# Kernel optimization log

Measured on AMD Instinct MI355X. Metric: run time of the kernel, lower is better.

Reference implementation:

```python
import jax, jax.numpy as jnp
import numpy as np
from jax.scipy.special import logsumexp

# Model config: alphabet='ACGTZY', collapse='ACGTCA' -> 4 canonical bases, 2 mods
NBASE = 4
NTRANS = 2 * NBASE * (NBASE + 1)          # 40 flip-flop transition states
CAN_NMODS = np.array([1, 1, 0, 0])        # mods per canonical base (A:Y, C:Z)
SIZE = NTRANS + 1 + int(CAN_NMODS.sum())  # 43 linear outputs
LARGE_LOG_VAL = np.float32(50000.0)
T, N, INSIZE = 2000, 128, 256


def _can_indices():
    """Per-canonical-base index groups into the mod block of the linear output."""
    idx, cur = [], 0
    for nm in CAN_NMODS:
        idx.append(np.concatenate([[0], np.arange(cur + 1, cur + 1 + nm)]))
        cur += nm
    return idx

CAN_INDICES = _can_indices()


def setup_inputs() -> dict:
    key = jax.random.key(0)
    k1, k2, k3 = jax.random.split(key, 3)
    x = jax.random.normal(k1, (T, N, INSIZE), dtype=jnp.float32)
    W = jax.random.normal(k2, (SIZE, INSIZE), dtype=jnp.float32) / np.float32(INSIZE ** 0.5)
    b = jax.random.normal(k3, (SIZE,), dtype=jnp.float32) * 0.1
    return {"x": x, "W": W, "b": b}


def global_norm_flipflop(scores):
    """Log-partition of the flip-flop CRF via a sequential log-space scan.

    scores: (T, N, 2*nbase*(nbase+1)).
    """
    Tn, Nn, _ = scores.shape
    # initial state: flip states uniform, flop states ~ -inf
    fwd0 = jnp.concatenate(
        [jnp.zeros((Nn, NBASE), scores.dtype),
         jnp.full((Nn, NBASE), -LARGE_LOG_VAL, scores.dtype)], axis=1)
    logZ0 = logsumexp(fwd0, axis=1, keepdims=True)
    fwd0 = fwd0 - logZ0

    def step(carry, scores_t):
        fwd, logZ = carry
        # (N, nbase+1, 2*nbase): dest-state x source-state transition scores
        curr = fwd[:, None, :] + scores_t.reshape(Nn, NBASE + 1, 2 * NBASE)
        base1 = logsumexp(curr[:, :NBASE], axis=2)                    # to-flip states
        base2 = jnp.logaddexp(curr[:, NBASE, :NBASE],
                              curr[:, NBASE, NBASE:])                 # to-flop (stay)
        new = jnp.concatenate([base1, base2], axis=1)                 # (N, 2*nbase)
        fac = logsumexp(new, axis=1, keepdims=True)
        return (new - fac, logZ + fac), None

    (_, logZ), _ = jax.lax.scan(step, (fwd0, logZ0), scores)
    return scores - logZ / np.float32(Tn)


def reference(x, W, b):
    # Linear projection: (T, N, insize) -> (T, N, size)
    y = jnp.einsum('tnf,cf->tnc', x, W) + b
    # Globally-normalized flip-flop transition scores
    trans = global_norm_flipflop(y[:, :, :NTRANS])
    # Per-canonical-base categorical (can + its mods) log-softmax scores
    mods = [jax.nn.log_softmax(y[:, :, NTRANS + idx], axis=2) for idx in CAN_INDICES]
    return jnp.concatenate([trans] + mods, axis=2)
```

## Files before the change

### kernel.cpp

```cpp
#include <hip/hip_runtime.h>

#define T_DIM 2000
#define N_DIM 128
#define IN_DIM 256
#define OUT_C 46
#define NROWS (T_DIM * N_DIM)
#define NCHUNK 250
#define CLEN 8
#define NSUPER 25
#define SLEN 10

typedef short bf16x8 __attribute__((ext_vector_type(8)));
typedef float f32x4 __attribute__((ext_vector_type(4)));

union F8U { bf16x8 v; uint32_t u[4]; };

__device__ __forceinline__ uint32_t cvtpk(float lo, float hi) {
  uint32_t r;
  asm("v_cvt_pk_bf16_f32 %0, %1, %2" : "=v"(r) : "v"(lo), "v"(hi));
  return r;
}

__device__ __forceinline__ float bf2f(unsigned short u) {
  uint32_t w = (uint32_t)u << 16;
  return __builtin_bit_cast(float, w);
}

#define LDSK 264

__global__ __launch_bounds__(256, 4) void k1_gemm(const float* __restrict__ x,
                                                  const float* __restrict__ W,
                                                  const float* __restrict__ b,
                                                  unsigned short* __restrict__ wsYT,
                                                  float* __restrict__ wsMod) {
  __shared__ unsigned short Wl[43 * LDSK];
  const int tid  = threadIdx.x;
  const int lane = tid & 63;
  const int wv   = tid >> 6;
  const int ln   = lane & 15;
  const int lh   = lane >> 4;

  {
    uint32_t* Wd = reinterpret_cast<uint32_t*>(Wl);
#pragma unroll
    for (int it = 0; it < 22; ++it) {
      int e = tid + it * 256;
      if (e < 43 * 128) {
        int n = e >> 7, kp = e & 127;
        float2 w = *reinterpret_cast<const float2*>(W + (size_t)n * IN_DIM + 2 * kp);
        Wd[n * (LDSK / 2) + kp] = cvtpk(w.x, w.y);
      }
    }
  }
  float bias[3];
#pragma unroll
  for (int nt = 0; nt < 3; ++nt) {
    int n = nt * 16 + ln;
    bias[nt] = b[n > 42 ? 42 : n];
  }
  __syncthreads();

  const int rowbase = blockIdx.x * 256 + wv * 64;
  const float* xbase = x + (size_t)(rowbase + ln) * IN_DIM + lh * 8;

  float4 bufA[8], bufB[8];
  f32x4 zero = {0.f, 0.f, 0.f, 0.f};
  f32x4 acc[3] = {zero, zero, zero};

#define LOADH(BUF, T, HF) do {                                               \
    const float* _p = xbase + (size_t)(T) * (16 * IN_DIM) + (HF) * 128;      \
    _Pragma("unroll")                                                        \
    for (int _s = 0; _s < 4; ++_s) {                                         \
      BUF[_s]     = *reinterpret_cast<const float4*>(_p + _s * 32);          \
      BUF[_s + 4] = *reinterpret_cast<const float4*>(_p + _s * 32 + 4);      \
    }                                                                        \
  } while (0)

#define COMPH(BUF, HF) do {                                                  \
    _Pragma("unroll")                                                        \
    for (int _s2 = 0; _s2 < 4; ++_s2) {                                      \
      F8U _af;                                                               \
      _af.u[0] = cvtpk(BUF[_s2].x, BUF[_s2].y);                              \
      _af.u[1] = cvtpk(BUF[_s2].z, BUF[_s2].w);                              \
      _af.u[2] = cvtpk(BUF[_s2 + 4].x, BUF[_s2 + 4].y);                      \
      _af.u[3] = cvtpk(BUF[_s2 + 4].z, BUF[_s2 + 4].w);                      \
      const int _s = (HF) * 4 + _s2;                                         \
      _Pragma("unroll")                                                      \
      for (int _nt = 0; _nt < 3; ++_nt) {                                    \
        const bf16x8 _bf = *reinterpret_cast<const bf16x8*>(                 \
            &Wl[(_nt * 16 + ln) * LDSK + _s * 32 + lh * 8]);                 \
        acc[_nt] = __builtin_amdgcn_mfma_f32_16x16x32_bf16(_af.v, _bf,       \
                                                           acc[_nt], 0, 0, 0);\
      }                                                                      \
    }                                                                        \
  } while (0)

  LOADH(bufA, 0, 0);
  LOADH(bufB, 0, 1);
#pragma unroll 1
  for (int t = 0; t < 4; ++t) {
    COMPH(bufA, 0);
    if (t < 3) LOADH(bufA, t + 1, 0);
    COMPH(bufB, 1);
    if (t < 3) LOADH(bufB, t + 1, 1);
    const int R0 = rowbase + t * 16;
    const int tt = R0 >> 7;
    const int n0 = (R0 & 127) + lh * 4;
#pragma unroll
    for (int nt = 0; nt < 3; ++nt) {
      const int c = nt * 16 + ln;
      if (nt < 2 || ln < 8) {
        uint32_t d0 = cvtpk(acc[nt][0] + bias[nt], acc[nt][1] + bias[nt]);
        uint32_t d1 = cvtpk(acc[nt][2] + bias[nt], acc[nt][3] + bias[nt]);
        uint2 v; v.x = d0; v.y = d1;
        *reinterpret_cast<uint2*>(wsYT + ((size_t)tt * 40 + c) * 128 + n0) = v;
      } else if (ln < 11) {
        float4 v;
        v.x = acc[2][0] + bias[2]; v.y = acc[2][1] + bias[2];
        v.z = acc[2][2] + bias[2]; v.w = acc[2][3] + bias[2];
        *reinterpret_cast<float4*>(
            wsMod + ((size_t)tt * 3 + (ln - 8)) * 128 + n0) = v;
      }
      acc[nt] = zero;
    }
  }
#undef LOADH
#undef COMPH
}

__global__ __launch_bounds__(256, 1) void k2a_chunk(const unsigned short* __restrict__ wsYT,
                                                    float* __restrict__ wsM,
                                                    float* __restrict__ wsScale) {
  const int g  = blockIdx.x * 256 + threadIdx.x;
  const int c  = g >> 7;
  const int n  = g & 127;
  const int t0 = c * CLEN;

  float M[8][8];
  float lsc = 0.f;
  float bufA[40], bufB[40];

#define LOADROW(BUF, TROW) do {                                              \
    const unsigned short* _yr = wsYT + (size_t)(TROW) * (40 * 128) + n;      \
    _Pragma("unroll")                                                        \
    for (int _q = 0; _q < 40; ++_q) BUF[_q] = bf2f(_yr[_q * 128]);           \
  } while (0)

#define INITM(BUF) do {                                                      \
    float _e[40];                                                            \
    _Pragma("unroll")                                                        \
    for (int _q = 0; _q < 40; ++_q) _e[_q] = __expf(BUF[_q]);                \
    _Pragma("unroll")                                                        \
    for (int _i = 0; _i < 4; ++_i)                                           \
      _Pragma("unroll")                                                      \
      for (int _j = 0; _j < 8; ++_j) M[_i][_j] = _e[8*_i+_j];                \
    _Pragma("unroll")                                                        \
    for (int _d = 0; _d < 4; ++_d) {                                         \
      _Pragma("unroll")                                                      \
      for (int _j = 0; _j < 8; ++_j) M[4+_d][_j] = 0.f;                      \
      M[4+_d][_d]   = _e[32+_d];                                             \
      M[4+_d][4+_d] = _e[36+_d];                                             \
    }                                                                        \
  } while (0)

#define STEPM(BUF) do {                                                      \
    float _e[40];                                                            \
    _Pragma("unroll")                                                        \
    for (int _q = 0; _q < 40; ++_q) _e[_q] = __expf(BUF[_q]);                \
    float _nm[8][8];                                                         \
    _Pragma("unroll")                                                        \
    for (int _j = 0; _j < 8; ++_j) {                                         \
      _Pragma("unroll")                                                      \
      for (int _i = 0; _i < 4; ++_i) {                                       \
        float _a = _e[8*_i+0]*M[0][_j] + _e[8*_i+1]*M[1][_j];                \
        float _b = _e[8*_i+2]*M[2][_j] + _e[8*_i+3]*M[3][_j];                \
        float _c = _e[8*_i+4]*M[4][_j] + _e[8*_i+5]*M[5][_j];                \
        float _d = _e[8*_i+6]*M[6][_j] + _e[8*_i+7]*M[7][_j];                \
        _nm[_i][_j] = (_a + _b) + (_c + _d);                                 \
      }                                                                      \
      _Pragma("unroll")                                                      \
      for (int _d2 = 0; _d2 < 4; ++_d2)                                      \
        _nm[4+_d2][_j] = _e[32+_d2]*M[_d2][_j] + _e[36+_d2]*M[4+_d2][_j];    \
    }                                                                        \
    _Pragma("unroll")                                                        \
    for (int _i = 0; _i < 8; ++_i)                                           \
      _Pragma("unroll")                                                      \
      for (int _j = 0; _j < 8; ++_j) M[_i][_j] = _nm[_i][_j];                \
  } while (0)

#define RENORM do {                                                          \
    float _S = 0.f;                                                          \
    _Pragma("unroll")                                                        \
    for (int _i = 0; _i < 8; ++_i)                                           \
      _Pragma("unroll")                                                      \
      for (int _j = 0; _j < 8; ++_j) _S += M[_i][_j];                        \
    lsc += __logf(_S);                                                       \
    const float _inv = 1.0f / _S;                                            \
    _Pragma("unroll")                                                        \
    for (int _i = 0; _i < 8; ++_i)                                           \
      _Pragma("unroll")                                                      \
      for (int _j = 0; _j < 8; ++_j) M[_i][_j] *= _inv;                      \
  } while (0)

  LOADROW(bufA, t0);
  LOADROW(bufB, t0 + 1);
  INITM(bufA);
  LOADROW(bufA, t0 + 2);
  STEPM(bufB);
  LOADROW(bufB, t0 + 3);
  STEPM(bufA);
  LOADROW(bufA, t0 + 4);
  STEPM(bufB);
  RENORM;
  LOADROW(bufB, t0 + 5);
  STEPM(bufA);
  LOADROW(bufA, t0 + 6);
  STEPM(bufB);
  LOADROW(bufB, t0 + 7);
  STEPM(bufA);
  STEPM(bufB);
  RENORM;

#undef LOADROW
#undef INITM
#undef STEPM
#undef RENORM

  float* dst = wsM + (size_t)(c * N_DIM + n) * 64;
#pragma unroll
  for (int q = 0; q < 16; ++q) {
    float4 v;
    v.x = M[q >> 1][(q & 1) * 4 + 0];
    v.y = M[q >> 1][(q & 1) * 4 + 1];
    v.z = M[q >> 1][(q & 1) * 4 + 2];
    v.w = M[q >> 1][(q & 1) * 4 + 3];
    reinterpret_cast<float4*>(dst)[q] = v;
  }
  wsScale[c * N_DIM + n] = lsc;
}

__global__ __launch_bounds__(128, 1) void k2c_super(const float* __restrict__ wsM,
                                                    const float* __restrict__ wsScale,
                                                    float* __restrict__ wsM2,
                                                    float* __restrict__ wsScale2) {
  const int sI = blockIdx.x;
  const int n  = threadIdx.x;
  const int c0 = sI * SLEN;

  float A[8][8], B0[8][8], B1[8][8];
  float lsc = 0.f;
#pragma unroll
  for (int u = 0; u < SLEN; ++u) lsc += wsScale[(c0 + u) * N_DIM + n];

#define LOADM(DST, CIDX) do {                                                \
    const float4* _p = reinterpret_cast<const float4*>(                      \
        wsM + (size_t)((CIDX) * N_DIM + n) * 64);                            \
    _Pragma("unroll")                                                        \
    for (int _q = 0; _q < 16; ++_q) {                                        \
      float4 _v = _p[_q];                                                    \
      DST[_q >> 1][(_q & 1) * 4 + 0] = _v.x;                                 \
      DST[_q >> 1][(_q & 1) * 4 + 1] = _v.y;                                 \
      DST[_q >> 1][(_q & 1) * 4 + 2] = _v.z;                                 \
      DST[_q >> 1][(_q & 1) * 4 + 3] = _v.w;                                 \
    }                                                                        \
  } while (0)

#define FOLD(BB) do {                                                        \
    float C[8][8];                                                           \
    _Pragma("unroll")                                                        \
    for (int _i = 0; _i < 8; ++_i)                                           \
      _Pragma("unroll")                                                      \
      for (int _j = 0; _j < 8; ++_j) {                                       \
        float _a = BB[_i][0]*A[0][_j] + BB[_i][1]*A[1][_j];                  \
        float _b = BB[_i][2]*A[2][_j] + BB[_i][3]*A[3][_j];                  \
        float _c = BB[_i][4]*A[4][_j] + BB[_i][5]*A[5][_j];                  \
        float _d = BB[_i][6]*A[6][_j] + BB[_i][7]*A[7][_j];                  \
        C[_i][_j] = (_a + _b) + (_c + _d);                                   \
      }                                                                      \
    float _S = 0.f;                                                          \
    _Pragma("unroll")                                                        \
    for (int _i = 0; _i < 8; ++_i)                                           \
      _Pragma("unroll")                                                      \
      for (int _j = 0; _j < 8; ++_j) _S += C[_i][_j];                        \
    lsc += __logf(_S);                                                       \
    const float _inv = 1.0f / _S;                                            \
    _Pragma("unroll")                                                        \
    for (int _i = 0; _i < 8; ++_i)                                           \
      _Pragma("unroll")                                                      \
      for (int _j = 0; _j < 8; ++_j) A[_i][_j] = C[_i][_j] * _inv;           \
  } while (0)

  LOADM(A, c0);
  LOADM(B0, c0 + 1);
  LOADM(B1, c0 + 2);
  FOLD(B0); LOADM(B0, c0 + 3);
  FOLD(B1); LOADM(B1, c0 + 4);
  FOLD(B0); LOADM(B0, c0 + 5);
  FOLD(B1); LOADM(B1, c0 + 6);
  FOLD(B0); LOADM(B0, c0 + 7);
  FOLD(B1); LOADM(B1, c0 + 8);
  FOLD(B0); LOADM(B0, c0 + 9);
  FOLD(B1);
  FOLD(B0);
#undef LOADM
#undef FOLD

  float* dst = wsM2 + (size_t)(sI * N_DIM + n) * 64;
#pragma unroll
  for (int q = 0; q < 16; ++q) {
    float4 v;
    v.x = A[q >> 1][(q & 1) * 4 + 0];
    v.y = A[q >> 1][(q & 1) * 4 + 1];
    v.z = A[q >> 1][(q & 1) * 4 + 2];
    v.w = A[q >> 1][(q & 1) * 4 + 3];
    reinterpret_cast<float4*>(dst)[q] = v;
  }
  wsScale2[sI * N_DIM + n] = lsc;
}

__global__ __launch_bounds__(128, 1) void k2b_fold(const float* __restrict__ wsM2,
                                                   const float* __restrict__ wsScale2,
                                                   float* __restrict__ wsLZ) {
  const int tid = threadIdx.x;
  const int n = blockIdx.x * 16 + (tid >> 3);
  const int i = tid & 7;
  const int gbase = (tid & 63) & ~7;

  float4 r0[NSUPER], r1[NSUPER];
  float sc[NSUPER];
#pragma unroll
  for (int s = 0; s < NSUPER; ++s) {
    const float* Mp = wsM2 + ((size_t)(s * N_DIM + n) * 64 + i * 8);
    r0[s] = *reinterpret_cast<const float4*>(Mp);
    r1[s] = *reinterpret_cast<const float4*>(Mp + 4);
    sc[s] = wsScale2[s * N_DIM + n];
  }

  float p[8] = {1.f, 1.f, 1.f, 1.f, 0.f, 0.f, 0.f, 0.f};
  float lz = 0.f;
#pragma unroll
  for (int s = 0; s < NSUPER; ++s) {
    float np = r0[s].x * p[0] + r0[s].y * p[1] + r0[s].z * p[2] + r0[s].w * p[3]
             + r1[s].x * p[4] + r1[s].y * p[5] + r1[s].z * p[6] + r1[s].w * p[7];
#pragma unroll
    for (int j = 0; j < 8; ++j) p[j] = __shfl(np, gbase + j, 64);
    float S = ((p[0] + p[1]) + (p[2] + p[3])) + ((p[4] + p[5]) + (p[6] + p[7]));
    lz += __logf(S) + sc[s];
    const float inv = 1.0f / S;
#pragma unroll
    for (int j = 0; j < 8; ++j) p[j] *= inv;
  }
  if (i == 0) wsLZ[n] = lz * (1.0f / (float)T_DIM);
}

__global__ __launch_bounds__(256, 3) void k3_out(const unsigned short* __restrict__ wsYT,
                                                 const float* __restrict__ wsMod,
                                                 const float* __restrict__ wsLZ,
                                                 float* __restrict__ out) {
  __shared__ float L[256 * 47];
  const int tid = threadIdx.x;
  const int fr  = blockIdx.x * 256 + tid;
  const int t   = fr >> 7;
  const int n   = fr & 127;
  const float sub = wsLZ[n];

  const unsigned short* yr = wsYT + (size_t)t * (40 * 128) + n;
  float* lrow = &L[tid * 47];
#pragma unroll
  for (int c = 0; c < 40; ++c) lrow[c] = bf2f(yr[c * 128]) - sub;

  const float* mp = wsMod + (size_t)t * (3 * 128) + n;
  const float y40 = mp[0], y41 = mp[128], y42 = mp[256];
  const float m01 = fmaxf(y40, y41);
  const float l01 = m01 + log1pf(__expf(fminf(y40, y41) - m01));
  const float m02 = fmaxf(y40, y42);
  const float l02 = m02 + log1pf(__expf(fminf(y40, y42) - m02));
  lrow[40] = y40 - l01;
  lrow[41] = y41 - l01;
  lrow[42] = y40 - l02;
  lrow[43] = y42 - l02;
  lrow[44] = 0.f;
  lrow[45] = 0.f;
  __syncthreads();

  const size_t base = (size_t)blockIdx.x * (256 * 46);
#pragma unroll
  for (int j = 0; j < 46; ++j) {
    const int e = j * 256 + tid;
    const int r = e / 46;
    const int c = e - r * 46;
    out[base + e] = L[r * 47 + c];
  }
}

extern "C" void kernel_launch(void* const* d_in, const int* in_sizes, int n_in,
                              void* d_out, int out_size, void* d_ws, size_t ws_size,
                              hipStream_t stream) {
  (void)in_sizes; (void)n_in; (void)out_size; (void)ws_size;
  const float* x = (const float*)d_in[0];
  const float* W = (const float*)d_in[1];
  const float* b = (const float*)d_in[2];
  float* out = (float*)d_out;

  char* wsb = (char*)d_ws;
  unsigned short* wsYT = (unsigned short*)wsb;
  float* wsMod   = (float*)(wsb + (size_t)T_DIM * 40 * 128 * 2);
  float* wsM     = wsMod + (size_t)T_DIM * 3 * N_DIM;
  float* wsScale = wsM + (size_t)NCHUNK * N_DIM * 64;
  float* wsM2    = wsScale + NCHUNK * N_DIM;
  float* wsScale2= wsM2 + (size_t)NSUPER * N_DIM * 64;
  float* wsLZ    = wsScale2 + NSUPER * N_DIM;

  hipLaunchKernelGGL(k1_gemm,   dim3(NROWS / 256), dim3(256), 0, stream,
                     x, W, b, wsYT, wsMod);
  hipLaunchKernelGGL(k2a_chunk, dim3(NCHUNK * N_DIM / 256), dim3(256), 0, stream,
                     wsYT, wsM, wsScale);
  hipLaunchKernelGGL(k2c_super, dim3(NSUPER), dim3(128), 0, stream,
                     wsM, wsScale, wsM2, wsScale2);
  hipLaunchKernelGGL(k2b_fold,  dim3(8), dim3(128), 0, stream,
                     wsM2, wsScale2, wsLZ);
  hipLaunchKernelGGL(k3_out,    dim3(NROWS / 256), dim3(256), 0, stream,
                     wsYT, wsMod, wsLZ, out);
}
```

Measured before the change: 116.1 us.

## Stage GEMM bf16 outputs in LDS for coalesced stores, reshape chunk grid, nontemporal output

```diff
diff --git a/kernel.cpp b/kernel.cpp
--- a/kernel.cpp
+++ b/kernel.cpp
@@ -27,13 +27,15 @@
 }
 
 #define LDSK 264
-
-__global__ __launch_bounds__(256, 4) void k1_gemm(const float* __restrict__ x,
+#define YPAD 132
+
+__global__ __launch_bounds__(256, 3) void k1_gemm(const float* __restrict__ x,
                                                   const float* __restrict__ W,
                                                   const float* __restrict__ b,
                                                   unsigned short* __restrict__ wsYT,
                                                   float* __restrict__ wsMod) {
   __shared__ unsigned short Wl[43 * LDSK];
+  __shared__ unsigned short Yst[2 * 40 * YPAD];
   const int tid  = threadIdx.x;
   const int lane = tid & 63;
   const int wv   = tid >> 6;
@@ -63,7 +65,7 @@
   const int rowbase = blockIdx.x * 256 + wv * 64;
   const float* xbase = x + (size_t)(rowbase + ln) * IN_DIM + lh * 8;
 
-  float4 bufA[8], bufB[8];
+  f32x4 bufA[8], bufB[8];
   f32x4 zero = {0.f, 0.f, 0.f, 0.f};
   f32x4 acc[3] = {zero, zero, zero};
 
@@ -71,8 +73,8 @@
     const float* _p = xbase + (size_t)(T) * (16 * IN_DIM) + (HF) * 128;      \
     _Pragma("unroll")                                                        \
     for (int _s = 0; _s < 4; ++_s) {                                         \
-      BUF[_s]     = *reinterpret_cast<const float4*>(_p + _s * 32);          \
-      BUF[_s + 4] = *reinterpret_cast<const float4*>(_p + _s * 32 + 4);      \
+      BUF[_s]     = *reinterpret_cast<const f32x4*>(_p + _s * 32);           \
+      BUF[_s + 4] = *reinterpret_cast<const f32x4*>(_p + _s * 32 + 4);       \
     }                                                                        \
   } while (0)
 
@@ -103,9 +105,9 @@
     if (t < 3) LOADH(bufA, t + 1, 0);
     COMPH(bufB, 1);
     if (t < 3) LOADH(bufB, t + 1, 1);
-    const int R0 = rowbase + t * 16;
-    const int tt = R0 >> 7;
-    const int n0 = (R0 & 127) + lh * 4;
+    const int R0   = rowbase + t * 16;
+    const int tloc = (R0 >> 7) & 1;
+    const int n0   = (R0 & 127) + lh * 4;
 #pragma unroll
     for (int nt = 0; nt < 3; ++nt) {
       const int c = nt * 16 + ln;
@@ -113,8 +115,9 @@
         uint32_t d0 = cvtpk(acc[nt][0] + bias[nt], acc[nt][1] + bias[nt]);
         uint32_t d1 = cvtpk(acc[nt][2] + bias[nt], acc[nt][3] + bias[nt]);
         uint2 v; v.x = d0; v.y = d1;
-        *reinterpret_cast<uint2*>(wsYT + ((size_t)tt * 40 + c) * 128 + n0) = v;
+        *reinterpret_cast<uint2*>(&Yst[(tloc * 40 + c) * YPAD + n0]) = v;
       } else if (ln < 11) {
+        const int tt = R0 >> 7;
         float4 v;
         v.x = acc[2][0] + bias[2]; v.y = acc[2][1] + bias[2];
         v.z = acc[2][2] + bias[2]; v.w = acc[2][3] + bias[2];
@@ -126,14 +129,24 @@
   }
 #undef LOADH
 #undef COMPH
-}
-
-__global__ __launch_bounds__(256, 1) void k2a_chunk(const unsigned short* __restrict__ wsYT,
+
+  __syncthreads();
+  uint2* gp = reinterpret_cast<uint2*>(wsYT + (size_t)blockIdx.x * (2 * 40 * 128));
+  const uint2* lp = reinterpret_cast<const uint2*>(Yst);
+#pragma unroll
+  for (int it = 0; it < 10; ++it) {
+    const int e   = tid + it * 256;
+    const int row = e >> 5;
+    const int q   = e & 31;
+    gp[e] = lp[row * 33 + q];
+  }
+}
+
+__global__ __launch_bounds__(128, 1) void k2a_chunk(const unsigned short* __restrict__ wsYT,
                                                     float* __restrict__ wsM,
                                                     float* __restrict__ wsScale) {
-  const int g  = blockIdx.x * 256 + threadIdx.x;
-  const int c  = g >> 7;
-  const int n  = g & 127;
+  const int c  = blockIdx.x;
+  const int n  = threadIdx.x;
   const int t0 = c * CLEN;
 
   float M[8][8];
@@ -389,7 +402,7 @@
     const int e = j * 256 + tid;
     const int r = e / 46;
     const int c = e - r * 46;
-    out[base + e] = L[r * 47 + c];
+    __builtin_nontemporal_store(L[r * 47 + c], &out[base + e]);
   }
 }
 
@@ -413,7 +426,7 @@
 
   hipLaunchKernelGGL(k1_gemm,   dim3(NROWS / 256), dim3(256), 0, stream,
                      x, W, b, wsYT, wsMod);
-  hipLaunchKernelGGL(k2a_chunk, dim3(NCHUNK * N_DIM / 256), dim3(256), 0, stream,
+  hipLaunchKernelGGL(k2a_chunk, dim3(NCHUNK), dim3(128), 0, stream,
                      wsYT, wsM, wsScale);
   hipLaunchKernelGGL(k2c_super, dim3(NSUPER), dim3(128), 0, stream,
                      wsM, wsScale, wsM2, wsScale2);
```

Measured after the change: 100.0 us. 13.8% less time.
